# Kernel tuning notes

Hardware: AMD Instinct MI355X
Metric: run time of the kernel (lower is better)

The kernel has to match this reference:

```python
import jax, jax.numpy as jnp
import numpy as np

N_NODES = 100000
N_EDGES = 1600000
EMB = 128
N_LAYERS = 3
BN_EPS = 1e-5


def setup_inputs() -> dict:
    key = jax.random.key(0)
    k1, k2, k3 = jax.random.split(key, 3)
    feats = jax.random.normal(k1, (N_NODES, EMB), dtype=jnp.float32)
    edge_index = jax.random.randint(k2, (2, N_EDGES), 0, N_NODES, dtype=jnp.int64)
    # Glorot-ish scaled weights per layer
    W = jax.random.normal(k3, (N_LAYERS, EMB, EMB), dtype=jnp.float32) * (1.0 / np.sqrt(EMB))
    b = jnp.zeros((N_LAYERS, EMB), dtype=jnp.float32)
    gamma = jnp.ones((N_LAYERS, EMB), dtype=jnp.float32)
    beta = jnp.zeros((N_LAYERS, EMB), dtype=jnp.float32)
    return {"feats": feats, "edge_index": edge_index, "W": W, "b": b, "gamma": gamma, "beta": beta}


def _gcn_layer(h, row, col, W_l, b_l):
    # GCNConv (add_self_loops=False, normalize=True): x = h @ W, symmetric-norm scatter-add, + bias
    x = h @ W_l  # [N, D]
    ones = jnp.ones((row.shape[0],), dtype=h.dtype)
    deg = jax.ops.segment_sum(ones, col, num_segments=N_NODES)  # in-degree of targets
    dinv = jnp.where(deg > 0, jax.lax.rsqrt(jnp.maximum(deg, 1.0)), 0.0)
    norm = dinv[row] * dinv[col]  # [E]
    msg = x[row] * norm[:, None]  # gather + scale, [E, D]
    out = jax.ops.segment_sum(msg, col, num_segments=N_NODES)  # scatter-add
    return out + b_l


def _batch_norm(h, gamma_l, beta_l):
    mu = jnp.mean(h, axis=0)
    var = jnp.mean(jnp.square(h - mu), axis=0)  # biased var (torch BN training math)
    return (h - mu) * jax.lax.rsqrt(var + BN_EPS) * gamma_l + beta_l


def reference(feats, edge_index, W, b, gamma, beta):
    row, col = edge_index[0], edge_index[1]  # source, target
    h = feats
    for l in range(N_LAYERS):
        h = _gcn_layer(h, row, col, W[l], b[l])
        h = _batch_norm(h, gamma[l], beta[l])
        # dropout treated as identity (eval mode); residual=False; JK='last'
    return h
```

## Files before the change

kernel.cpp:

```cpp
#include <hip/hip_runtime.h>
#include <cstdint>
#include <cstddef>

#define BN_EPS 1e-5f
#define NCHUNK 256

typedef short bf16x8 __attribute__((ext_vector_type(8)));
typedef float f32x4 __attribute__((ext_vector_type(4)));


__device__ __forceinline__ int edge_at(const void* e, long long i, int m64) {
  return m64 ? (int)((const long long*)e)[i] : ((const int*)e)[i];
}

__device__ __forceinline__ unsigned short f2bf(float f) {
  unsigned int u = __float_as_uint(f);
  unsigned int r = (u + 0x7FFFu + ((u >> 16) & 1u)) >> 16;
  return (unsigned short)r;
}

__device__ __forceinline__ unsigned int pack2bf(float lo, float hi) {
  return (unsigned int)f2bf(lo) | ((unsigned int)f2bf(hi) << 16);
}

__global__ void detect_kernel(const int* __restrict__ e, int* __restrict__ mode) {
  int nz = 0;
  for (int i = 1; i < 512; i += 2) nz |= e[i];
  mode[0] = (nz == 0) ? 1 : 0;
}


__global__ __launch_bounds__(256) void count_kernel(const void* __restrict__ edges,
                                                    const int* __restrict__ mode,
                                                    int* __restrict__ blockcounts,
                                                    int E, int nb, int chunk) {
  __shared__ int h[1024];
  int m = mode[0];
  for (int i = threadIdx.x; i < nb; i += 256) h[i] = 0;
  __syncthreads();
  long long lo = (long long)blockIdx.x * chunk;
  long long hi = lo + chunk;
  if (hi > E) hi = E;
  for (long long i = lo + threadIdx.x; i < hi; i += 256) {
    int c = edge_at(edges, (long long)E + i, m);
    atomicAdd(&h[c >> 8], 1);
  }
  __syncthreads();
  for (int j = threadIdx.x; j < nb; j += 256)
    blockcounts[(size_t)j * NCHUNK + blockIdx.x] = h[j];
}

__global__ __launch_bounds__(256) void scan1_kernel(const int* __restrict__ src,
                                                    int* __restrict__ tprefix,
                                                    int* __restrict__ bsum, int n) {
  __shared__ int s[256];
  int t = threadIdx.x;
  int gid = blockIdx.x * 256 + t;
  int base = gid * 4;
  int sum = 0;
#pragma unroll
  for (int j = 0; j < 4; j++) {
    int i = base + j;
    if (i < n) sum += src[i];
  }
  s[t] = sum;
  __syncthreads();
  for (int off = 1; off < 256; off <<= 1) {
    int v = (t >= off) ? s[t - off] : 0;
    __syncthreads();
    s[t] += v;
    __syncthreads();
  }
  tprefix[gid] = s[t] - sum;
  if (t == 255) bsum[blockIdx.x] = s[255];
}

__global__ __launch_bounds__(256) void scan2_kernel(int* __restrict__ bsum, int nbk,
                                                    int* __restrict__ out, int n) {
  __shared__ int s[256];
  int t = threadIdx.x;
  int v = (t < nbk) ? bsum[t] : 0;
  s[t] = v;
  __syncthreads();
  for (int off = 1; off < 256; off <<= 1) {
    int u = (t >= off) ? s[t - off] : 0;
    __syncthreads();
    s[t] += u;
    __syncthreads();
  }
  if (t < nbk) bsum[t] = s[t] - v;
  if (t == 255) out[n] = s[255];
}

__global__ __launch_bounds__(256) void scan3_kernel(const int* __restrict__ src,
                                                    const int* __restrict__ tprefix,
                                                    const int* __restrict__ bsum,
                                                    int* __restrict__ out, int n) {
  int gid = blockIdx.x * 256 + threadIdx.x;
  int run = bsum[blockIdx.x] + tprefix[gid];
  int base = gid * 4;
#pragma unroll
  for (int j = 0; j < 4; j++) {
    int i = base + j;
    if (i < n) {
      int c = src[i];
      out[i] = run;
      run += c;
    }
  }
}

__global__ __launch_bounds__(256) void scatter_kernel(const void* __restrict__ edges,
                                                      const int* __restrict__ mode,
                                                      const int* __restrict__ moff,
                                                      int* __restrict__ pairs,
                                                      int E, int nb, int chunk) {
  __shared__ int cur[1024];
  int m = mode[0];
  for (int j = threadIdx.x; j < nb; j += 256)
    cur[j] = moff[(size_t)j * NCHUNK + blockIdx.x];
  __syncthreads();
  long long lo = (long long)blockIdx.x * chunk;
  long long hi = lo + chunk;
  if (hi > E) hi = E;
  for (long long i = lo + threadIdx.x; i < hi; i += 256) {
    int r = edge_at(edges, i, m);
    int c = edge_at(edges, (long long)E + i, m);
    int pos = atomicAdd(&cur[c >> 8], 1);
    pairs[pos] = (r << 8) | (c & 255);
  }
}

__global__ __launch_bounds__(256) void passB1_kernel(const int* __restrict__ pairs,
                                                     const int* __restrict__ moff,
                                                     int* __restrict__ deg,
                                                     float* __restrict__ dinv, int n) {
  __shared__ int h[256];
  int b = blockIdx.x;
  h[threadIdx.x] = 0;
  __syncthreads();
  int lo = moff[(size_t)b * NCHUNK];
  int hi = moff[(size_t)(b + 1) * NCHUNK];
  for (int e = lo + threadIdx.x; e < hi; e += 256)
    atomicAdd(&h[pairs[e] & 255], 1);
  __syncthreads();
  int node = b * 256 + threadIdx.x;
  if (node < n) {
    int d = h[threadIdx.x];
    deg[node] = d;
    dinv[node] = d > 0 ? rsqrtf((float)d) : 0.f;
  }
}

__global__ __launch_bounds__(256) void passB2_kernel(const int* __restrict__ pairs,
                                                     const int* __restrict__ moff,
                                                     const int* __restrict__ offsets,
                                                     int* __restrict__ csr_row, int n) {
  __shared__ int cur[256];
  int b = blockIdx.x;
  int node = b * 256 + threadIdx.x;
  cur[threadIdx.x] = (node < n) ? offsets[node] : 0;
  __syncthreads();
  int lo = moff[(size_t)b * NCHUNK];
  int hi = moff[(size_t)(b + 1) * NCHUNK];
  for (int e = lo + threadIdx.x; e < hi; e += 256) {
    int p = pairs[e];
    int pos = atomicAdd(&cur[p & 255], 1);
    csr_row[pos] = p >> 8;
  }
}

__global__ __launch_bounds__(256) void prepWR_kernel(const float* __restrict__ W,
                                                     const float* __restrict__ scale,
                                                     const float* __restrict__ shift,
                                                     int use_affine,
                                                     unsigned short* __restrict__ Wt,
                                                     float* __restrict__ rbias) {
  int idx = blockIdx.x * 256 + threadIdx.x;
  int nc = idx >> 7, k = idx & 127;
  float v = W[(size_t)k * 128 + nc];
  if (use_affine) v *= scale[k];
  Wt[(size_t)nc * 128 + k] = f2bf(v);
  if (blockIdx.x == 0 && threadIdx.x < 128) {
    int c = threadIdx.x;
    float s = 0.f;
    if (use_affine) {
      for (int kk = 0; kk < 128; kk++) s += shift[kk] * W[(size_t)kk * 128 + c];
    }
    rbias[c] = s;
  }
}

template <int A_IS_FP32>
__global__ __launch_bounds__(256) void gemm_mfma_kernel(
    const void* __restrict__ Ain, const unsigned short* __restrict__ Wt,
    const float* __restrict__ rbias, const float* __restrict__ dinv,
    unsigned short* __restrict__ xb, int n) {
  int l = threadIdx.x & 63;
  int w = threadIdx.x >> 6;
  int row0 = blockIdx.x * 64 + w * 16;
  int am = row0 + (l & 15);
  int amc = am < n ? am : n - 1;
  int kg = l >> 4;

  f32x4 acc[8];
#pragma unroll
  for (int nt = 0; nt < 8; nt++) {
    f32x4 zv = {0.f, 0.f, 0.f, 0.f};
    acc[nt] = zv;
  }

#pragma unroll
  for (int kk = 0; kk < 4; kk++) {
    bf16x8 a;
    if (A_IS_FP32) {
      const float* ap = (const float*)Ain + (size_t)amc * 128 + kk * 32 + kg * 8;
      float4 f0 = *(const float4*)ap;
      float4 f1 = *(const float4*)(ap + 4);
      a[0] = (short)f2bf(f0.x); a[1] = (short)f2bf(f0.y);
      a[2] = (short)f2bf(f0.z); a[3] = (short)f2bf(f0.w);
      a[4] = (short)f2bf(f1.x); a[5] = (short)f2bf(f1.y);
      a[6] = (short)f2bf(f1.z); a[7] = (short)f2bf(f1.w);
    } else {
      a = *(const bf16x8*)((const unsigned short*)Ain + (size_t)amc * 128 + kk * 32 + kg * 8);
    }
#pragma unroll
    for (int nt = 0; nt < 8; nt++) {
      bf16x8 b = *(const bf16x8*)(Wt + (size_t)(nt * 16 + (l & 15)) * 128 + kk * 32 + kg * 8);
      acc[nt] = __builtin_amdgcn_mfma_f32_16x16x32_bf16(a, b, acc[nt], 0, 0, 0);
    }
  }

  int col0 = l & 15;
  int rbase = row0 + (l >> 4) * 4;
  float dv[4];
#pragma unroll
  for (int r = 0; r < 4; r++) {
    int rr = rbase + r;
    dv[r] = dinv[rr < n ? rr : n - 1];
  }
#pragma unroll
  for (int nt = 0; nt < 8; nt++) {
    float rb = rbias[nt * 16 + col0];
#pragma unroll
    for (int r = 0; r < 4; r++) {
      int rr = rbase + r;
      if (rr < n)
        xb[(size_t)rr * 128 + nt * 16 + col0] = f2bf((acc[nt][r] + rb) * dv[r]);
    }
  }
}

template <int F32OUT>
__global__ __launch_bounds__(256) void agg_kernel(
    const uint4* __restrict__ x4, const int* __restrict__ csr_row,
    const int* __restrict__ offsets, const float* __restrict__ dinv,
    void* __restrict__ z, int n) {
  int node = blockIdx.x * 16 + (threadIdx.x >> 4);
  int d8 = threadIdx.x & 15;
  if (node >= n) return;
  int lo = offsets[node], hi = offsets[node + 1];
  float a0[8] = {}, a1[8] = {}, a2[8] = {}, a3[8] = {};
#define ACC8(A, v)                                                         \
  A[0] += __uint_as_float((v).x << 16); A[1] += __uint_as_float((v).x & 0xffff0000u); \
  A[2] += __uint_as_float((v).y << 16); A[3] += __uint_as_float((v).y & 0xffff0000u); \
  A[4] += __uint_as_float((v).z << 16); A[5] += __uint_as_float((v).z & 0xffff0000u); \
  A[6] += __uint_as_float((v).w << 16); A[7] += __uint_as_float((v).w & 0xffff0000u);
  int e = lo;
  for (; e + 4 <= hi; e += 4) {
    int r0 = csr_row[e];
    int r1 = csr_row[e + 1];
    int r2 = csr_row[e + 2];
    int r3 = csr_row[e + 3];
    uint4 v0 = x4[(size_t)r0 * 16 + d8];
    uint4 v1 = x4[(size_t)r1 * 16 + d8];
    uint4 v2 = x4[(size_t)r2 * 16 + d8];
    uint4 v3 = x4[(size_t)r3 * 16 + d8];
    ACC8(a0, v0) ACC8(a1, v1) ACC8(a2, v2) ACC8(a3, v3)
  }
  for (; e < hi; e++) {
    uint4 v = x4[(size_t)csr_row[e] * 16 + d8];
    ACC8(a0, v)
  }
#undef ACC8
  float dvn = dinv[node];
  float s[8];
#pragma unroll
  for (int j = 0; j < 8; j++) s[j] = (a0[j] + a1[j] + a2[j] + a3[j]) * dvn;
  if (F32OUT) {
    float* zp = (float*)z + (size_t)node * 128 + d8 * 8;
    *(float4*)zp = make_float4(s[0], s[1], s[2], s[3]);
    *(float4*)(zp + 4) = make_float4(s[4], s[5], s[6], s[7]);
  } else {
    uint4 o = make_uint4(pack2bf(s[0], s[1]), pack2bf(s[2], s[3]),
                         pack2bf(s[4], s[5]), pack2bf(s[6], s[7]));
    *(uint4*)((unsigned short*)z + (size_t)node * 128 + d8 * 8) = o;
  }
}

template <int F32IN>
__global__ __launch_bounds__(256) void stats2_kernel(
    const void* __restrict__ z, float* __restrict__ partial, int total8) {
  __shared__ float ps[256];
  int t = threadIdx.x;
  ps[t] = 0.f;
  __syncthreads();
  int d8 = t & 15;
  float s[8] = {}, q[8] = {};
  int idx = blockIdx.x * 256 + t;
  int stride = gridDim.x * 256;
  for (int i = idx; i < total8; i += stride) {
    float v[8];
    if (F32IN) {
      const float* zp = (const float*)z + (size_t)i * 8;
      float4 f0 = *(const float4*)zp;
      float4 f1 = *(const float4*)(zp + 4);
      v[0] = f0.x; v[1] = f0.y; v[2] = f0.z; v[3] = f0.w;
      v[4] = f1.x; v[5] = f1.y; v[6] = f1.z; v[7] = f1.w;
    } else {
      uint4 u = ((const uint4*)z)[i];
      v[0] = __uint_as_float(u.x << 16); v[1] = __uint_as_float(u.x & 0xffff0000u);
      v[2] = __uint_as_float(u.y << 16); v[3] = __uint_as_float(u.y & 0xffff0000u);
      v[4] = __uint_as_float(u.z << 16); v[5] = __uint_as_float(u.z & 0xffff0000u);
      v[6] = __uint_as_float(u.w << 16); v[7] = __uint_as_float(u.w & 0xffff0000u);
    }
#pragma unroll
    for (int j = 0; j < 8; j++) { s[j] += v[j]; q[j] += v[j] * v[j]; }
  }
#pragma unroll
  for (int j = 0; j < 8; j++) {
    atomicAdd(&ps[d8 * 8 + j], s[j]);
    atomicAdd(&ps[128 + d8 * 8 + j], q[j]);
  }
  __syncthreads();
  partial[(size_t)blockIdx.x * 256 + t] = ps[t];
}

__global__ __launch_bounds__(256) void reduce_stats_kernel(
    const float* __restrict__ partial, float* __restrict__ out, int nblk) {
  __shared__ float red[256];
  int c = blockIdx.x;
  float s = 0.f;
  for (int i = threadIdx.x; i < nblk; i += 256) s += partial[(size_t)i * 256 + c];
  red[threadIdx.x] = s;
  __syncthreads();
  for (int o = 128; o > 0; o >>= 1) {
    if (threadIdx.x < o) red[threadIdx.x] += red[threadIdx.x + o];
    __syncthreads();
  }
  if (threadIdx.x == 0) out[c] = red[0];
}

__global__ void finalize_kernel(const float* __restrict__ colsum,
                                const float* __restrict__ colsumsq,
                                const float* __restrict__ gamma,
                                const float* __restrict__ beta,
                                float* __restrict__ scale, float* __restrict__ shift,
                                float invN) {
  int d = threadIdx.x;
  float mu = colsum[d] * invN;
  float var = colsumsq[d] * invN - mu * mu;
  var = fmaxf(var, 0.f);
  float sc = gamma[d] * rsqrtf(var + BN_EPS);
  scale[d] = sc;
  shift[d] = beta[d] - mu * sc;
}

__global__ __launch_bounds__(256) void norm_kernel(
    float* __restrict__ z, const float* __restrict__ scale,
    const float* __restrict__ shift, int total4) {
  int idx = blockIdx.x * blockDim.x + threadIdx.x;
  int stride = gridDim.x * blockDim.x;
  for (int i = idx; i < total4; i += stride) {
    float4 v = ((const float4*)z)[i];
    int d0 = (i & 31) * 4;
    v.x = v.x * scale[d0] + shift[d0];
    v.y = v.y * scale[d0 + 1] + shift[d0 + 1];
    v.z = v.z * scale[d0 + 2] + shift[d0 + 2];
    v.w = v.w * scale[d0 + 3] + shift[d0 + 3];
    ((float4*)z)[i] = v;
  }
}


extern "C" void kernel_launch(void* const* d_in, const int* in_sizes, int n_in,
                              void* d_out, int out_size, void* d_ws, size_t ws_size,
                              hipStream_t stream) {
  const float* feats = (const float*)d_in[0];
  const void* edges = d_in[1];
  const float* W = (const float*)d_in[2];
  const float* gamma = (const float*)d_in[4];
  const float* beta = (const float*)d_in[5];

  const int n = in_sizes[0] / 128;
  const int E = in_sizes[1] / 2;

  const int nb = (n + 255) / 256;
  const int m = nb * NCHUNK;
  const int chunk = (E + NCHUNK - 1) / NCHUNK;
  const int sb_n = (n + 1023) / 1024;
  const int sb_m = (m + 1023) / 1024;
  const int sb_max = sb_n > sb_m ? sb_n : sb_m;
  const int nagg = (n + 15) / 16;
  const int nstat = 1024;

  char* ws = (char*)d_ws;
  size_t off = 0;
  unsigned short* xb = (unsigned short*)(ws + off); off += (size_t)n * 128 * 2; off = (off + 255) & ~(size_t)255;
  int* deg = (int*)(ws + off); off += (size_t)n * 4;
  float* dinv = (float*)(ws + off); off += (size_t)n * 4;
  int* offsets = (int*)(ws + off); off += (size_t)(n + 1) * 4; off = (off + 255) & ~(size_t)255;
  int* csr_row = (int*)(ws + off); off += (size_t)E * 4; off = (off + 255) & ~(size_t)255;
  int* pairs = (int*)(ws + off); off += (size_t)E * 4; off = (off + 255) & ~(size_t)255;
  int* blockcounts = (int*)(ws + off); off += (size_t)m * 4; off = (off + 255) & ~(size_t)255;
  int* moff = (int*)(ws + off); off += (size_t)(m + 1) * 4; off = (off + 255) & ~(size_t)255;
  int* tprefix = (int*)(ws + off); off += (size_t)sb_max * 256 * 4; off = (off + 255) & ~(size_t)255;
  int* bsum = (int*)(ws + off); off += 256 * 4;
  unsigned short* Wt = (unsigned short*)(ws + off); off += 128 * 128 * 2; off = (off + 255) & ~(size_t)255;
  float* rbias = (float*)(ws + off); off += 128 * 4;
  float* colsum = (float*)(ws + off); off += 128 * 4;
  float* colsumsq = (float*)(ws + off); off += 128 * 4;
  float* scale = (float*)(ws + off); off += 128 * 4;
  float* shift = (float*)(ws + off); off += 128 * 4;
  int* mode = (int*)(ws + off); off += 4;

  float* partial = (float*)pairs;

  detect_kernel<<<1, 1, 0, stream>>>((const int*)edges, mode);
  count_kernel<<<NCHUNK, 256, 0, stream>>>(edges, mode, blockcounts, E, nb, chunk);
  scan1_kernel<<<sb_m, 256, 0, stream>>>(blockcounts, tprefix, bsum, m);
  scan2_kernel<<<1, 256, 0, stream>>>(bsum, sb_m, moff, m);
  scan3_kernel<<<sb_m, 256, 0, stream>>>(blockcounts, tprefix, bsum, moff, m);
  scatter_kernel<<<NCHUNK, 256, 0, stream>>>(edges, mode, moff, pairs, E, nb, chunk);
  passB1_kernel<<<nb, 256, 0, stream>>>(pairs, moff, deg, dinv, n);
  scan1_kernel<<<sb_n, 256, 0, stream>>>(deg, tprefix, bsum, n);
  scan2_kernel<<<1, 256, 0, stream>>>(bsum, sb_n, offsets, n);
  scan3_kernel<<<sb_n, 256, 0, stream>>>(deg, tprefix, bsum, offsets, n);
  passB2_kernel<<<nb, 256, 0, stream>>>(pairs, moff, offsets, csr_row, n);

  unsigned short* zb = (unsigned short*)d_out;
  float* zf = (float*)d_out;
  const int ggrid = (n + 63) / 64;
  const int total8 = n * 16;

  for (int l = 0; l < 3; l++) {
    prepWR_kernel<<<64, 256, 0, stream>>>(W + (size_t)l * 16384, scale, shift,
                                          l > 0 ? 1 : 0, Wt, rbias);
    if (l == 0)
      gemm_mfma_kernel<1><<<ggrid, 256, 0, stream>>>(feats, Wt, rbias, dinv, xb, n);
    else
      gemm_mfma_kernel<0><<<ggrid, 256, 0, stream>>>(zb, Wt, rbias, dinv, xb, n);
    if (l < 2) {
      agg_kernel<0><<<nagg, 256, 0, stream>>>(
          (const uint4*)xb, csr_row, offsets, dinv, zb, n);
      stats2_kernel<0><<<nstat, 256, 0, stream>>>(zb, partial, total8);
    } else {
      agg_kernel<1><<<nagg, 256, 0, stream>>>(
          (const uint4*)xb, csr_row, offsets, dinv, zf, n);
      stats2_kernel<1><<<nstat, 256, 0, stream>>>(zf, partial, total8);
    }
    reduce_stats_kernel<<<256, 256, 0, stream>>>(partial, colsum, nstat);
    finalize_kernel<<<1, 128, 0, stream>>>(colsum, colsumsq, gamma + l * 128,
                                           beta + l * 128, scale, shift, 1.0f / (float)n);
  }
  norm_kernel<<<2048, 256, 0, stream>>>(zf, scale, shift, (n * 128) / 4);
}
```

Before: 498.2 us.

## Fuse CSR build passes, fold BN finalize into consumers, unroll aggregation by eight

The degree-count and CSR-fill passes become one kernel that computes node offsets with an in-block prefix scan, removing the three global scan launches and the deg buffer. The BN finalize kernel is removed, and scale and shift are now recomputed from the column stats inside prepWR and norm. The aggregation loop gets an 8-way unroll and a launch-bounds occupancy hint. The aim is fewer launches and more memory-level parallelism in the gather, at the cost of higher register pressure in agg_kernel.

```diff
diff --git a/kernel.cpp b/kernel.cpp
--- a/kernel.cpp
+++ b/kernel.cpp
@@ -131,63 +131,78 @@
   }
 }
 
-__global__ __launch_bounds__(256) void passB1_kernel(const int* __restrict__ pairs,
-                                                     const int* __restrict__ moff,
-                                                     int* __restrict__ deg,
-                                                     float* __restrict__ dinv, int n) {
+__global__ __launch_bounds__(256) void passB12_kernel(const int* __restrict__ pairs,
+                                                      const int* __restrict__ moff,
+                                                      float* __restrict__ dinv,
+                                                      int* __restrict__ offsets,
+                                                      int* __restrict__ csr_row, int n) {
   __shared__ int h[256];
+  __shared__ int s[256];
+  int t = threadIdx.x;
   int b = blockIdx.x;
-  h[threadIdx.x] = 0;
+  h[t] = 0;
   __syncthreads();
   int lo = moff[(size_t)b * NCHUNK];
   int hi = moff[(size_t)(b + 1) * NCHUNK];
-  for (int e = lo + threadIdx.x; e < hi; e += 256)
+  for (int e = lo + t; e < hi; e += 256)
     atomicAdd(&h[pairs[e] & 255], 1);
   __syncthreads();
-  int node = b * 256 + threadIdx.x;
+  int d = h[t];
+  s[t] = d;
+  __syncthreads();
+  for (int off = 1; off < 256; off <<= 1) {
+    int v = (t >= off) ? s[t - off] : 0;
+    __syncthreads();
+    s[t] += v;
+    __syncthreads();
+  }
+  int start = lo + s[t] - d;
+  int node = b * 256 + t;
   if (node < n) {
-    int d = h[threadIdx.x];
-    deg[node] = d;
+    offsets[node] = start;
     dinv[node] = d > 0 ? rsqrtf((float)d) : 0.f;
-  }
-}
-
-__global__ __launch_bounds__(256) void passB2_kernel(const int* __restrict__ pairs,
-                                                     const int* __restrict__ moff,
-                                                     const int* __restrict__ offsets,
-                                                     int* __restrict__ csr_row, int n) {
-  __shared__ int cur[256];
-  int b = blockIdx.x;
-  int node = b * 256 + threadIdx.x;
-  cur[threadIdx.x] = (node < n) ? offsets[node] : 0;
-  __syncthreads();
-  int lo = moff[(size_t)b * NCHUNK];
-  int hi = moff[(size_t)(b + 1) * NCHUNK];
-  for (int e = lo + threadIdx.x; e < hi; e += 256) {
+    if (node == n - 1) offsets[n] = hi;
+  }
+  s[t] = start;
+  __syncthreads();
+  for (int e = lo + t; e < hi; e += 256) {
     int p = pairs[e];
-    int pos = atomicAdd(&cur[p & 255], 1);
+    int pos = atomicAdd(&s[p & 255], 1);
     csr_row[pos] = p >> 8;
   }
 }
 
 __global__ __launch_bounds__(256) void prepWR_kernel(const float* __restrict__ W,
-                                                     const float* __restrict__ scale,
-                                                     const float* __restrict__ shift,
-                                                     int use_affine,
+                                                     const float* __restrict__ colstats,
+                                                     const float* __restrict__ gamma,
+                                                     const float* __restrict__ beta,
+                                                     float invN, int use_affine,
                                                      unsigned short* __restrict__ Wt,
                                                      float* __restrict__ rbias) {
-  int idx = blockIdx.x * 256 + threadIdx.x;
+  __shared__ float sc[128], sh[128];
+  int t = threadIdx.x;
+  if (t < 128) {
+    float scv = 1.f, shv = 0.f;
+    if (use_affine) {
+      float mu = colstats[t] * invN;
+      float var = colstats[128 + t] * invN - mu * mu;
+      var = fmaxf(var, 0.f);
+      scv = gamma[t] * rsqrtf(var + BN_EPS);
+      shv = beta[t] - mu * scv;
+    }
+    sc[t] = scv;
+    sh[t] = shv;
+  }
+  __syncthreads();
+  int idx = blockIdx.x * 256 + t;
   int nc = idx >> 7, k = idx & 127;
-  float v = W[(size_t)k * 128 + nc];
-  if (use_affine) v *= scale[k];
-  Wt[(size_t)nc * 128 + k] = f2bf(v);
-  if (blockIdx.x == 0 && threadIdx.x < 128) {
-    int c = threadIdx.x;
+  Wt[(size_t)nc * 128 + k] = f2bf(W[(size_t)k * 128 + nc] * sc[k]);
+  if (blockIdx.x == 0 && t < 128) {
     float s = 0.f;
     if (use_affine) {
-      for (int kk = 0; kk < 128; kk++) s += shift[kk] * W[(size_t)kk * 128 + c];
-    }
-    rbias[c] = s;
+      for (int kk = 0; kk < 128; kk++) s += sh[kk] * W[(size_t)kk * 128 + t];
+    }
+    rbias[t] = s;
   }
 }
 
@@ -252,7 +267,7 @@
 }
 
 template <int F32OUT>
-__global__ __launch_bounds__(256) void agg_kernel(
+__global__ __launch_bounds__(256, 4) void agg_kernel(
     const uint4* __restrict__ x4, const int* __restrict__ csr_row,
     const int* __restrict__ offsets, const float* __restrict__ dinv,
     void* __restrict__ z, int n) {
@@ -267,6 +282,26 @@
   A[4] += __uint_as_float((v).z << 16); A[5] += __uint_as_float((v).z & 0xffff0000u); \
   A[6] += __uint_as_float((v).w << 16); A[7] += __uint_as_float((v).w & 0xffff0000u);
   int e = lo;
+  for (; e + 8 <= hi; e += 8) {
+    int r0 = csr_row[e];
+    int r1 = csr_row[e + 1];
+    int r2 = csr_row[e + 2];
+    int r3 = csr_row[e + 3];
+    int r4 = csr_row[e + 4];
+    int r5 = csr_row[e + 5];
+    int r6 = csr_row[e + 6];
+    int r7 = csr_row[e + 7];
+    uint4 v0 = x4[(size_t)r0 * 16 + d8];
+    uint4 v1 = x4[(size_t)r1 * 16 + d8];
+    uint4 v2 = x4[(size_t)r2 * 16 + d8];
+    uint4 v3 = x4[(size_t)r3 * 16 + d8];
+    uint4 v4 = x4[(size_t)r4 * 16 + d8];
+    uint4 v5 = x4[(size_t)r5 * 16 + d8];
+    uint4 v6 = x4[(size_t)r6 * 16 + d8];
+    uint4 v7 = x4[(size_t)r7 * 16 + d8];
+    ACC8(a0, v0) ACC8(a1, v1) ACC8(a2, v2) ACC8(a3, v3)
+    ACC8(a0, v4) ACC8(a1, v5) ACC8(a2, v6) ACC8(a3, v7)
+  }
   for (; e + 4 <= hi; e += 4) {
     int r0 = csr_row[e];
     int r1 = csr_row[e + 1];
@@ -351,33 +386,30 @@
   if (threadIdx.x == 0) out[c] = red[0];
 }
 
-__global__ void finalize_kernel(const float* __restrict__ colsum,
-                                const float* __restrict__ colsumsq,
-                                const float* __restrict__ gamma,
-                                const float* __restrict__ beta,
-                                float* __restrict__ scale, float* __restrict__ shift,
-                                float invN) {
-  int d = threadIdx.x;
-  float mu = colsum[d] * invN;
-  float var = colsumsq[d] * invN - mu * mu;
-  var = fmaxf(var, 0.f);
-  float sc = gamma[d] * rsqrtf(var + BN_EPS);
-  scale[d] = sc;
-  shift[d] = beta[d] - mu * sc;
-}
-
 __global__ __launch_bounds__(256) void norm_kernel(
-    float* __restrict__ z, const float* __restrict__ scale,
-    const float* __restrict__ shift, int total4) {
-  int idx = blockIdx.x * blockDim.x + threadIdx.x;
+    float* __restrict__ z, const float* __restrict__ colstats,
+    const float* __restrict__ gamma, const float* __restrict__ beta,
+    float invN, int total4) {
+  __shared__ float sc[128], sh[128];
+  int t = threadIdx.x;
+  if (t < 128) {
+    float mu = colstats[t] * invN;
+    float var = colstats[128 + t] * invN - mu * mu;
+    var = fmaxf(var, 0.f);
+    float s = gamma[t] * rsqrtf(var + BN_EPS);
+    sc[t] = s;
+    sh[t] = beta[t] - mu * s;
+  }
+  __syncthreads();
+  int idx = blockIdx.x * blockDim.x + t;
   int stride = gridDim.x * blockDim.x;
   for (int i = idx; i < total4; i += stride) {
     float4 v = ((const float4*)z)[i];
     int d0 = (i & 31) * 4;
-    v.x = v.x * scale[d0] + shift[d0];
-    v.y = v.y * scale[d0 + 1] + shift[d0 + 1];
-    v.z = v.z * scale[d0 + 2] + shift[d0 + 2];
-    v.w = v.w * scale[d0 + 3] + shift[d0 + 3];
+    v.x = v.x * sc[d0] + sh[d0];
+    v.y = v.y * sc[d0 + 1] + sh[d0 + 1];
+    v.z = v.z * sc[d0 + 2] + sh[d0 + 2];
+    v.w = v.w * sc[d0 + 3] + sh[d0 + 3];
     ((float4*)z)[i] = v;
   }
 }
@@ -398,30 +430,24 @@
   const int nb = (n + 255) / 256;
   const int m = nb * NCHUNK;
   const int chunk = (E + NCHUNK - 1) / NCHUNK;
-  const int sb_n = (n + 1023) / 1024;
   const int sb_m = (m + 1023) / 1024;
-  const int sb_max = sb_n > sb_m ? sb_n : sb_m;
   const int nagg = (n + 15) / 16;
   const int nstat = 1024;
 
   char* ws = (char*)d_ws;
   size_t off = 0;
   unsigned short* xb = (unsigned short*)(ws + off); off += (size_t)n * 128 * 2; off = (off + 255) & ~(size_t)255;
-  int* deg = (int*)(ws + off); off += (size_t)n * 4;
   float* dinv = (float*)(ws + off); off += (size_t)n * 4;
   int* offsets = (int*)(ws + off); off += (size_t)(n + 1) * 4; off = (off + 255) & ~(size_t)255;
   int* csr_row = (int*)(ws + off); off += (size_t)E * 4; off = (off + 255) & ~(size_t)255;
   int* pairs = (int*)(ws + off); off += (size_t)E * 4; off = (off + 255) & ~(size_t)255;
   int* blockcounts = (int*)(ws + off); off += (size_t)m * 4; off = (off + 255) & ~(size_t)255;
   int* moff = (int*)(ws + off); off += (size_t)(m + 1) * 4; off = (off + 255) & ~(size_t)255;
-  int* tprefix = (int*)(ws + off); off += (size_t)sb_max * 256 * 4; off = (off + 255) & ~(size_t)255;
+  int* tprefix = (int*)(ws + off); off += (size_t)sb_m * 256 * 4; off = (off + 255) & ~(size_t)255;
   int* bsum = (int*)(ws + off); off += 256 * 4;
   unsigned short* Wt = (unsigned short*)(ws + off); off += 128 * 128 * 2; off = (off + 255) & ~(size_t)255;
   float* rbias = (float*)(ws + off); off += 128 * 4;
-  float* colsum = (float*)(ws + off); off += 128 * 4;
-  float* colsumsq = (float*)(ws + off); off += 128 * 4;
-  float* scale = (float*)(ws + off); off += 128 * 4;
-  float* shift = (float*)(ws + off); off += 128 * 4;
+  float* colstats = (float*)(ws + off); off += 256 * 4;
   int* mode = (int*)(ws + off); off += 4;
 
   float* partial = (float*)pairs;
@@ -432,19 +458,17 @@
   scan2_kernel<<<1, 256, 0, stream>>>(bsum, sb_m, moff, m);
   scan3_kernel<<<sb_m, 256, 0, stream>>>(blockcounts, tprefix, bsum, moff, m);
   scatter_kernel<<<NCHUNK, 256, 0, stream>>>(edges, mode, moff, pairs, E, nb, chunk);
-  passB1_kernel<<<nb, 256, 0, stream>>>(pairs, moff, deg, dinv, n);
-  scan1_kernel<<<sb_n, 256, 0, stream>>>(deg, tprefix, bsum, n);
-  scan2_kernel<<<1, 256, 0, stream>>>(bsum, sb_n, offsets, n);
-  scan3_kernel<<<sb_n, 256, 0, stream>>>(deg, tprefix, bsum, offsets, n);
-  passB2_kernel<<<nb, 256, 0, stream>>>(pairs, moff, offsets, csr_row, n);
+  passB12_kernel<<<nb, 256, 0, stream>>>(pairs, moff, dinv, offsets, csr_row, n);
 
   unsigned short* zb = (unsigned short*)d_out;
   float* zf = (float*)d_out;
   const int ggrid = (n + 63) / 64;
   const int total8 = n * 16;
+  const float invN = 1.0f / (float)n;
 
   for (int l = 0; l < 3; l++) {
-    prepWR_kernel<<<64, 256, 0, stream>>>(W + (size_t)l * 16384, scale, shift,
+    prepWR_kernel<<<64, 256, 0, stream>>>(W + (size_t)l * 16384, colstats,
+                                          gamma + l * 128, beta + l * 128, invN,
                                           l > 0 ? 1 : 0, Wt, rbias);
     if (l == 0)
       gemm_mfma_kernel<1><<<ggrid, 256, 0, stream>>>(feats, Wt, rbias, dinv, xb, n);
@@ -459,9 +483,8 @@
           (const uint4*)xb, csr_row, offsets, dinv, zf, n);
       stats2_kernel<1><<<nstat, 256, 0, stream>>>(zf, partial, total8);
     }
-    reduce_stats_kernel<<<256, 256, 0, stream>>>(partial, colsum, nstat);
-    finalize_kernel<<<1, 128, 0, stream>>>(colsum, colsumsq, gamma + l * 128,
-                                           beta + l * 128, scale, shift, 1.0f / (float)n);
-  }
-  norm_kernel<<<2048, 256, 0, stream>>>(zf, scale, shift, (n * 128) / 4);
-}
+    reduce_stats_kernel<<<256, 256, 0, stream>>>(partial, colstats, nstat);
+  }
+  norm_kernel<<<2048, 256, 0, stream>>>(zf, colstats, gamma + 2 * 128, beta + 2 * 128,
+                                        invN, (n * 128) / 4);
+}
```

Result: faster. 485.1 us (-2.6%).
